# Kernel optimization log

Hardware: AMD Instinct MI355X
Metric: run time of the kernel (lower is better)

The kernel has to match this reference:

```python
import jax, jax.numpy as jnp
import numpy as np

N = 50000
E = 400000
IN_C, HID, OUT2, NCLS = 128, 512, 64, 2
NEG_SLOPE = 0.2


def setup_inputs() -> dict:
    key = jax.random.key(0)
    ks = jax.random.split(key, 12)
    x = jax.random.normal(ks[0], (N, IN_C), dtype=jnp.float32)
    edge_index = jax.random.randint(ks[1], (2, E), 0, N, dtype=jnp.int64)
    def glorot(k, shape):
        fan_in = shape[0]
        return jax.random.normal(k, shape, dtype=jnp.float32) / np.float32(np.sqrt(fan_in))
    return {
        "x": x,
        "edge_index": edge_index,
        "W1": glorot(ks[2], (IN_C, HID)),
        "a1_src": glorot(ks[3], (HID,)),
        "a1_dst": glorot(ks[4], (HID,)),
        "b1": jnp.zeros((HID,), jnp.float32),
        "W2": glorot(ks[5], (HID, OUT2)),
        "a2_src": glorot(ks[6], (OUT2,)),
        "a2_dst": glorot(ks[7], (OUT2,)),
        "b2": jnp.zeros((OUT2,), jnp.float32),
        "fcW": glorot(ks[8], (OUT2, NCLS)),
        "fcb": jnp.zeros((NCLS,), jnp.float32),
    }


def _gat_conv(h_in, src, dst, W, a_src, a_dst, b):
    # single-head GATConv (PyG defaults: heads=1, negative_slope=0.2, self-loops already added)
    h = h_in @ W                                   # [N, D]
    alpha_s = h @ a_src                            # [N]
    alpha_d = h @ a_dst                            # [N]
    e = jax.nn.leaky_relu(alpha_s[src] + alpha_d[dst], NEG_SLOPE)  # [E']
    # segment softmax over incoming edges of each dst node
    m = jax.ops.segment_max(e, dst, num_segments=N)
    ex = jnp.exp(e - m[dst])
    denom = jax.ops.segment_sum(ex, dst, num_segments=N)
    alpha = ex / denom[dst]                        # [E']
    out = jax.ops.segment_sum(alpha[:, None] * h[src], dst, num_segments=N)
    return out + b


def reference(x, edge_index, W1, a1_src, a1_dst, b1, W2, a2_src, a2_dst, b2, fcW, fcb):
    loops = jnp.arange(N, dtype=edge_index.dtype)
    src = jnp.concatenate([edge_index[0], loops])  # add self loops (PyG default)
    dst = jnp.concatenate([edge_index[1], loops])
    h = jax.nn.relu(_gat_conv(x, src, dst, W1, a1_src, a1_dst, b1))
    h = jax.nn.relu(_gat_conv(h, src, dst, W2, a2_src, a2_dst, b2))
    # F.dropout(training=self.training): identity in eval mode
    return h @ fcW + fcb
```

## Files before the change

### kernel.cpp

```cpp
#include <hip/hip_runtime.h>

#define N_NODES 50000
#define N_EDGES 400000
#define E_TOT   (N_EDGES + N_NODES)
#define IN_C 128
#define HID  512
#define OUT2 64
#define NEG_SLOPE 0.2f

typedef short bf16x8 __attribute__((ext_vector_type(8)));
typedef float f32x4  __attribute__((ext_vector_type(4)));

__device__ __forceinline__ float wave_sum(float v) {
#pragma unroll
  for (int o = 32; o > 0; o >>= 1) v += __shfl_xor(v, o, 64);
  return v;
}
__device__ __forceinline__ int wave_sum_i(int v) {
#pragma unroll
  for (int o = 32; o > 0; o >>= 1) v += __shfl_xor(v, o, 64);
  return v;
}
__device__ __forceinline__ float wave_max(float v) {
#pragma unroll
  for (int o = 32; o > 0; o >>= 1) v = fmaxf(v, __shfl_xor(v, o, 64));
  return v;
}
__device__ __forceinline__ float leaky(float t) {
  return (t > 0.f) ? t : NEG_SLOPE * t;
}

__device__ __forceinline__ unsigned short bf16_rne(float x) {
  unsigned u = __float_as_uint(x);
  u += 0x7fffu + ((u >> 16) & 1u);
  return (unsigned short)(u >> 16);
}
__device__ __forceinline__ void split_bf16(float x, unsigned short& h, unsigned short& l) {
  h = bf16_rne(x);
  float hf = __uint_as_float(((unsigned)h) << 16);
  l = bf16_rne(x - hf);
}

__device__ __forceinline__ int esrc(const int* __restrict__ ei, int e) {
  return (e < N_EDGES) ? ei[e] : (e - N_EDGES);
}
__device__ __forceinline__ int edst(const int* __restrict__ ei, int e) {
  return (e < N_EDGES) ? ei[N_EDGES + e] : (e - N_EDGES);
}

__global__ void count_deg(const int* __restrict__ ei, int* __restrict__ deg) {
  int e = blockIdx.x * blockDim.x + threadIdx.x;
  if (e >= E_TOT) return;
  atomicAdd(&deg[edst(ei, e)], 1);
}

__global__ void scanA(const int* __restrict__ deg, int* __restrict__ bsum) {
  __shared__ int ws[16];
  int t = threadIdx.x, lane = t & 63, w = t >> 6;
  int i = blockIdx.x * 1024 + t;
  int v = (i < N_NODES) ? deg[i] : 0;
  int s = wave_sum_i(v);
  if (lane == 0) ws[w] = s;
  __syncthreads();
  if (t == 0) {
    int tot = 0;
#pragma unroll
    for (int k = 0; k < 16; k++) tot += ws[k];
    bsum[blockIdx.x] = tot;
  }
}

__global__ void scanB(const int* __restrict__ bsum, int* __restrict__ boff, int nb) {
  int lane = threadIdx.x;
  int v = (lane < nb) ? bsum[lane] : 0;
  int sc = v;
#pragma unroll
  for (int off = 1; off < 64; off <<= 1) {
    int u = __shfl_up(sc, off, 64);
    if (lane >= off) sc += u;
  }
  if (lane < nb) boff[lane] = sc - v;
}

__global__ void scanC(const int* __restrict__ deg, const int* __restrict__ boff,
                      int* __restrict__ row_ptr) {
  __shared__ int ws[16];
  int t = threadIdx.x, lane = t & 63, w = t >> 6;
  int i = blockIdx.x * 1024 + t;
  int v = (i < N_NODES) ? deg[i] : 0;
  int sc = v;
#pragma unroll
  for (int off = 1; off < 64; off <<= 1) {
    int u = __shfl_up(sc, off, 64);
    if (lane >= off) sc += u;
  }
  if (lane == 63) ws[w] = sc;
  __syncthreads();
  if (w == 0 && lane < 16) {
    int u = ws[lane];
#pragma unroll
    for (int off = 1; off < 16; off <<= 1) {
      int uu = __shfl_up(u, off, 64);
      if (lane >= off) u += uu;
    }
    ws[lane] = u;
  }
  __syncthreads();
  int excl = ((w > 0) ? ws[w - 1] : 0) + boff[blockIdx.x];
  if (i < N_NODES) row_ptr[i + 1] = sc + excl;
  if (blockIdx.x == 0 && t == 0) row_ptr[0] = 0;
}

__global__ void fill_csr(const int* __restrict__ ei, const int* __restrict__ row_ptr,
                         int* __restrict__ cursor, int* __restrict__ csr_src) {
  int e = blockIdx.x * blockDim.x + threadIdx.x;
  if (e >= E_TOT) return;
  int d = edst(ei, e);
  int pos = atomicAdd(&cursor[d], 1);
  csr_src[row_ptr[d] + pos] = esrc(ei, e);
}

__global__ void prep_weights(const float* __restrict__ W1, const float* __restrict__ W2,
                             const float* __restrict__ a1s, const float* __restrict__ a1d,
                             unsigned short* __restrict__ W1F, unsigned short* __restrict__ W2F,
                             float* __restrict__ w1s, float* __restrict__ w1d) {
  int b = blockIdx.x;
  if (b < 32) {
    int t = b * 256 + threadIdx.x;
    int fi = t >> 6, l = t & 63;
    int ks = fi & 3, n = (fi >> 2) & 3, jt = fi >> 4;
    int col = jt * 64 + n * 16 + (l & 15);
    int k0 = ks * 32 + (l >> 4) * 8;
    unsigned short hv[8], lv[8];
#pragma unroll
    for (int e = 0; e < 8; e++)
      split_bf16(W1[(size_t)(k0 + e) * HID + col], hv[e], lv[e]);
    unsigned short* ph = W1F + ((size_t)(fi * 2 + 0) * 64 + l) * 8;
    unsigned short* pl = W1F + ((size_t)(fi * 2 + 1) * 64 + l) * 8;
#pragma unroll
    for (int e = 0; e < 8; e++) { ph[e] = hv[e]; pl[e] = lv[e]; }
  } else if (b < 48) {
    int t = (b - 32) * 256 + threadIdx.x;
    int fi = t >> 6, l = t & 63;
    int n = fi & 3, ks = (fi >> 2) & 1, jt = fi >> 3;
    int col = n * 16 + (l & 15);
    int k0 = jt * 64 + ks * 32 + (l >> 4) * 8;
    unsigned short hv[8], lv[8];
#pragma unroll
    for (int e = 0; e < 8; e++)
      split_bf16(W2[(size_t)(k0 + e) * OUT2 + col], hv[e], lv[e]);
    unsigned short* ph = W2F + ((size_t)(fi * 2 + 0) * 64 + l) * 8;
    unsigned short* pl = W2F + ((size_t)(fi * 2 + 1) * 64 + l) * 8;
#pragma unroll
    for (int e = 0; e < 8; e++) { ph[e] = hv[e]; pl[e] = lv[e]; }
  } else {
    int wid = ((b - 48) * 256 + threadIdx.x) >> 6;
    int lane = threadIdx.x & 63;
    if (wid >= IN_C) return;
    const float* row = W1 + (size_t)wid * HID;
    float s = 0.f, d = 0.f;
#pragma unroll
    for (int j0 = 0; j0 < HID; j0 += 64) {
      float w = row[j0 + lane];
      s += w * a1s[j0 + lane];
      d += w * a1d[j0 + lane];
    }
    s = wave_sum(s); d = wave_sum(d);
    if (lane == 0) { w1s[wid] = s; w1d[wid] = d; }
  }
}

__global__ void node_scores128(const float* __restrict__ x, const float* __restrict__ ws,
                               const float* __restrict__ wd, float* __restrict__ as_,
                               float* __restrict__ ad_) {
  int wid = (blockIdx.x * blockDim.x + threadIdx.x) >> 6;
  int lane = threadIdx.x & 63;
  if (wid >= N_NODES) return;
  float2 v = ((const float2*)(x + (size_t)wid * IN_C))[lane];
  float2 w1 = ((const float2*)ws)[lane];
  float2 w2 = ((const float2*)wd)[lane];
  float s = wave_sum(v.x * w1.x + v.y * w1.y);
  float d = wave_sum(v.x * w2.x + v.y * w2.y);
  if (lane == 0) { as_[wid] = s; ad_[wid] = d; }
}

__global__ void sm_agg1(const int* __restrict__ row_ptr, const int* __restrict__ csr_src,
                        const float* __restrict__ as_, const float* __restrict__ ad_,
                        const float* __restrict__ x, float* __restrict__ xa) {
  int wid = (blockIdx.x * blockDim.x + threadIdx.x) >> 6;
  int lane = threadIdx.x & 63;
  if (wid >= N_NODES) return;
  int beg = row_ptr[wid], end = row_ptr[wid + 1];
  int deg = end - beg;
  float adv = ad_[wid];
  const float2* x2 = (const float2*)x;
  float2 acc = make_float2(0.f, 0.f);
  if (deg <= 64) {
    int s = 0; float sc = -3.4e38f;
    if (lane < deg) { s = csr_src[beg + lane]; sc = leaky(as_[s] + adv); }
    float m = wave_max(sc);
    float ex = (lane < deg) ? __expf(sc - m) : 0.f;
    float sum = wave_sum(ex);
    float a = ex / sum;
    int kk = 0;
    for (; kk + 8 <= deg; kk += 8) {
      float w0 = __shfl(a, kk, 64),     w1 = __shfl(a, kk + 1, 64);
      float w2 = __shfl(a, kk + 2, 64), w3 = __shfl(a, kk + 3, 64);
      float w4 = __shfl(a, kk + 4, 64), w5 = __shfl(a, kk + 5, 64);
      float w6 = __shfl(a, kk + 6, 64), w7 = __shfl(a, kk + 7, 64);
      int s0 = __shfl(s, kk, 64),     s1 = __shfl(s, kk + 1, 64);
      int s2 = __shfl(s, kk + 2, 64), s3 = __shfl(s, kk + 3, 64);
      int s4 = __shfl(s, kk + 4, 64), s5 = __shfl(s, kk + 5, 64);
      int s6 = __shfl(s, kk + 6, 64), s7 = __shfl(s, kk + 7, 64);
      float2 r0 = x2[(size_t)s0 * 64 + lane];
      float2 r1 = x2[(size_t)s1 * 64 + lane];
      float2 r2 = x2[(size_t)s2 * 64 + lane];
      float2 r3 = x2[(size_t)s3 * 64 + lane];
      float2 r4 = x2[(size_t)s4 * 64 + lane];
      float2 r5 = x2[(size_t)s5 * 64 + lane];
      float2 r6 = x2[(size_t)s6 * 64 + lane];
      float2 r7 = x2[(size_t)s7 * 64 + lane];
      acc.x += w0 * r0.x + w1 * r1.x + w2 * r2.x + w3 * r3.x
             + w4 * r4.x + w5 * r5.x + w6 * r6.x + w7 * r7.x;
      acc.y += w0 * r0.y + w1 * r1.y + w2 * r2.y + w3 * r3.y
             + w4 * r4.y + w5 * r5.y + w6 * r6.y + w7 * r7.y;
    }
    for (; kk + 4 <= deg; kk += 4) {
      float w0 = __shfl(a, kk, 64),     w1 = __shfl(a, kk + 1, 64);
      float w2 = __shfl(a, kk + 2, 64), w3 = __shfl(a, kk + 3, 64);
      int s0 = __shfl(s, kk, 64),     s1 = __shfl(s, kk + 1, 64);
      int s2 = __shfl(s, kk + 2, 64), s3 = __shfl(s, kk + 3, 64);
      float2 r0 = x2[(size_t)s0 * 64 + lane];
      float2 r1 = x2[(size_t)s1 * 64 + lane];
      float2 r2 = x2[(size_t)s2 * 64 + lane];
      float2 r3 = x2[(size_t)s3 * 64 + lane];
      acc.x += w0 * r0.x + w1 * r1.x + w2 * r2.x + w3 * r3.x;
      acc.y += w0 * r0.y + w1 * r1.y + w2 * r2.y + w3 * r3.y;
    }
    for (; kk < deg; kk++) {
      float w = __shfl(a, kk, 64);
      int sv = __shfl(s, kk, 64);
      float2 r = x2[(size_t)sv * 64 + lane];
      acc.x += w * r.x; acc.y += w * r.y;
    }
  } else {
    float m = -3.4e38f;
    for (int k = beg + lane; k < end; k += 64)
      m = fmaxf(m, leaky(as_[csr_src[k]] + adv));
    m = wave_max(m);
    float sum = 0.f;
    for (int k = beg + lane; k < end; k += 64)
      sum += __expf(leaky(as_[csr_src[k]] + adv) - m);
    sum = wave_sum(sum);
    float inv = 1.f / sum;
    for (int k = beg; k < end; k++) {
      int sv = csr_src[k];
      float w = __expf(leaky(as_[sv] + adv) - m) * inv;
      float2 r = x2[(size_t)sv * 64 + lane];
      acc.x += w * r.x; acc.y += w * r.y;
    }
  }
  ((float2*)(xa + (size_t)wid * IN_C))[lane] = acc;
}

__launch_bounds__(128, 2)
__global__ void fused_gemm_mfma(const float* __restrict__ xa,
                                const unsigned short* __restrict__ W1F,
                                const float* __restrict__ b1,
                                const unsigned short* __restrict__ W2F,
                                const float* __restrict__ a2s, const float* __restrict__ a2d,
                                float* __restrict__ h2, float* __restrict__ as2,
                                float* __restrict__ ad2) {
  __shared__ unsigned int TS[64][64];
  int t = threadIdx.x;
  int w = t >> 6;
  int l = t & 63;
  int lr = l & 15;
  int G  = l >> 4;
  int base = blockIdx.x * 64 + w * 32;

  bf16x8 aFh[2][4], aFl[2][4];
#pragma unroll
  for (int m = 0; m < 2; m++) {
    int grow = base + m * 16 + lr;
    bool ok = (grow < N_NODES);
    const float* rp = xa + (size_t)grow * IN_C;
#pragma unroll
    for (int ks = 0; ks < 4; ks++) {
      float4 v0 = make_float4(0.f, 0.f, 0.f, 0.f), v1 = v0;
      if (ok) {
        v0 = *(const float4*)(rp + ks * 32 + G * 8);
        v1 = *(const float4*)(rp + ks * 32 + G * 8 + 4);
      }
      unsigned short h, lo;
      split_bf16(v0.x, h, lo); aFh[m][ks][0] = (short)h; aFl[m][ks][0] = (short)lo;
      split_bf16(v0.y, h, lo); aFh[m][ks][1] = (short)h; aFl[m][ks][1] = (short)lo;
      split_bf16(v0.z, h, lo); aFh[m][ks][2] = (short)h; aFl[m][ks][2] = (short)lo;
      split_bf16(v0.w, h, lo); aFh[m][ks][3] = (short)h; aFl[m][ks][3] = (short)lo;
      split_bf16(v1.x, h, lo); aFh[m][ks][4] = (short)h; aFl[m][ks][4] = (short)lo;
      split_bf16(v1.y, h, lo); aFh[m][ks][5] = (short)h; aFl[m][ks][5] = (short)lo;
      split_bf16(v1.z, h, lo); aFh[m][ks][6] = (short)h; aFl[m][ks][6] = (short)lo;
      split_bf16(v1.w, h, lo); aFh[m][ks][7] = (short)h; aFl[m][ks][7] = (short)lo;
    }
  }

  const bf16x8* W1Fv = (const bf16x8*)W1F;
  const bf16x8* W2Fv = (const bf16x8*)W2F;

  f32x4 acc2[2][4];
#pragma unroll
  for (int m = 0; m < 2; m++)
#pragma unroll
    for (int n = 0; n < 4; n++) acc2[m][n] = (f32x4){0.f, 0.f, 0.f, 0.f};

  for (int jt = 0; jt < 8; jt++) {
    bf16x8 w2h[2][4], w2l[2][4];
#pragma unroll
    for (int ks = 0; ks < 2; ks++)
#pragma unroll
      for (int n = 0; n < 4; n++) {
        int fi2 = (jt * 2 + ks) * 4 + n;
        w2h[ks][n] = W2Fv[(size_t)(fi2 * 2 + 0) * 64 + l];
        w2l[ks][n] = W2Fv[(size_t)(fi2 * 2 + 1) * 64 + l];
      }
    f32x4 acc1[2][4];
#pragma unroll
    for (int m = 0; m < 2; m++)
#pragma unroll
      for (int n = 0; n < 4; n++) acc1[m][n] = (f32x4){0.f, 0.f, 0.f, 0.f};
#pragma unroll
    for (int ks = 0; ks < 4; ks++) {
      bf16x8 bh[4], bl[4];
#pragma unroll
      for (int n = 0; n < 4; n++) {
        int fi = (jt * 4 + n) * 4 + ks;
        bh[n] = W1Fv[(size_t)(fi * 2 + 0) * 64 + l];
        bl[n] = W1Fv[(size_t)(fi * 2 + 1) * 64 + l];
      }
#pragma unroll
      for (int n = 0; n < 4; n++) {
#pragma unroll
        for (int m = 0; m < 2; m++) {
          acc1[m][n] = __builtin_amdgcn_mfma_f32_16x16x32_bf16(aFh[m][ks], bh[n], acc1[m][n], 0, 0, 0);
          acc1[m][n] = __builtin_amdgcn_mfma_f32_16x16x32_bf16(aFl[m][ks], bh[n], acc1[m][n], 0, 0, 0);
          acc1[m][n] = __builtin_amdgcn_mfma_f32_16x16x32_bf16(aFh[m][ks], bl[n], acc1[m][n], 0, 0, 0);
        }
      }
    }
#pragma unroll
    for (int n = 0; n < 4; n++) {
      float bv = b1[jt * 64 + n * 16 + lr];
#pragma unroll
      for (int m = 0; m < 2; m++) {
#pragma unroll
        for (int r = 0; r < 4; r++) {
          float vv = fmaxf(acc1[m][n][r] + bv, 0.f);
          unsigned short hh, ll;
          split_bf16(vv, hh, ll);
          int rowL = w * 32 + m * 16 + G * 4 + r;
          int colS = (n * 16 + lr) ^ ((rowL & 7) << 2);
          TS[rowL][colS] = (unsigned)hh | ((unsigned)ll << 16);
        }
      }
    }
#pragma unroll
    for (int ks = 0; ks < 2; ks++) {
      int kl = ks * 32 + G * 8;
      bf16x8 a2h[2], a2l[2];
#pragma unroll
      for (int m = 0; m < 2; m++) {
        int rowA = w * 32 + m * 16 + lr;
        int sw2 = (rowA & 7) << 2;
        uint4 q0 = *(const uint4*)&TS[rowA][(kl + 0) ^ sw2];
        uint4 q1 = *(const uint4*)&TS[rowA][(kl + 4) ^ sw2];
        a2h[m][0] = (short)(q0.x & 0xffff); a2l[m][0] = (short)(q0.x >> 16);
        a2h[m][1] = (short)(q0.y & 0xffff); a2l[m][1] = (short)(q0.y >> 16);
        a2h[m][2] = (short)(q0.z & 0xffff); a2l[m][2] = (short)(q0.z >> 16);
        a2h[m][3] = (short)(q0.w & 0xffff); a2l[m][3] = (short)(q0.w >> 16);
        a2h[m][4] = (short)(q1.x & 0xffff); a2l[m][4] = (short)(q1.x >> 16);
        a2h[m][5] = (short)(q1.y & 0xffff); a2l[m][5] = (short)(q1.y >> 16);
        a2h[m][6] = (short)(q1.z & 0xffff); a2l[m][6] = (short)(q1.z >> 16);
        a2h[m][7] = (short)(q1.w & 0xffff); a2l[m][7] = (short)(q1.w >> 16);
      }
#pragma unroll
      for (int n = 0; n < 4; n++) {
#pragma unroll
        for (int m = 0; m < 2; m++) {
          acc2[m][n] = __builtin_amdgcn_mfma_f32_16x16x32_bf16(a2h[m], w2h[ks][n], acc2[m][n], 0, 0, 0);
          acc2[m][n] = __builtin_amdgcn_mfma_f32_16x16x32_bf16(a2l[m], w2h[ks][n], acc2[m][n], 0, 0, 0);
          acc2[m][n] = __builtin_amdgcn_mfma_f32_16x16x32_bf16(a2h[m], w2l[ks][n], acc2[m][n], 0, 0, 0);
        }
      }
    }
  }

#pragma unroll
  for (int m = 0; m < 2; m++) {
#pragma unroll
    for (int r = 0; r < 4; r++) {
      int grow = base + m * 16 + G * 4 + r;
      if (grow < N_NODES) {
#pragma unroll
        for (int n = 0; n < 4; n++)
          h2[(size_t)grow * OUT2 + n * 16 + lr] = acc2[m][n][r];
      }
      float sp = 0.f, dp = 0.f;
#pragma unroll
      for (int n = 0; n < 4; n++) {
        float v = acc2[m][n][r];
        sp += v * a2s[n * 16 + lr];
        dp += v * a2d[n * 16 + lr];
      }
#pragma unroll
      for (int o = 1; o < 16; o <<= 1) {
        sp += __shfl_xor(sp, o, 64);
        dp += __shfl_xor(dp, o, 64);
      }
      if (lr == 0 && grow < N_NODES) { as2[grow] = sp; ad2[grow] = dp; }
    }
  }
}

__global__ void sm_agg2_final(const int* __restrict__ row_ptr, const int* __restrict__ csr_src,
                              const float* __restrict__ as_, const float* __restrict__ ad_,
                              const float* __restrict__ h2, const float* __restrict__ b2,
                              const float* __restrict__ fcW, const float* __restrict__ fcb,
                              float* __restrict__ out) {
  int wid = (blockIdx.x * blockDim.x + threadIdx.x) >> 6;
  int lane = threadIdx.x & 63;
  if (wid >= N_NODES) return;
  int beg = row_ptr[wid], end = row_ptr[wid + 1];
  int deg = end - beg;
  float adv = ad_[wid];
  float acc = 0.f;
  if (deg <= 64) {
    int s = 0; float sc = -3.4e38f;
    if (lane < deg) { s = csr_src[beg + lane]; sc = leaky(as_[s] + adv); }
    float m = wave_max(sc);
    float ex = (lane < deg) ? __expf(sc - m) : 0.f;
    float sum = wave_sum(ex);
    float a = ex / sum;
    int kk = 0;
    for (; kk + 8 <= deg; kk += 8) {
      float w0 = __shfl(a, kk, 64),     w1 = __shfl(a, kk + 1, 64);
      float w2 = __shfl(a, kk + 2, 64), w3 = __shfl(a, kk + 3, 64);
      float w4 = __shfl(a, kk + 4, 64), w5 = __shfl(a, kk + 5, 64);
      float w6 = __shfl(a, kk + 6, 64), w7 = __shfl(a, kk + 7, 64);
      int s0 = __shfl(s, kk, 64),     s1 = __shfl(s, kk + 1, 64);
      int s2 = __shfl(s, kk + 2, 64), s3 = __shfl(s, kk + 3, 64);
      int s4 = __shfl(s, kk + 4, 64), s5 = __shfl(s, kk + 5, 64);
      int s6 = __shfl(s, kk + 6, 64), s7 = __shfl(s, kk + 7, 64);
      float r0 = h2[(size_t)s0 * OUT2 + lane];
      float r1 = h2[(size_t)s1 * OUT2 + lane];
      float r2 = h2[(size_t)s2 * OUT2 + lane];
      float r3 = h2[(size_t)s3 * OUT2 + lane];
      float r4 = h2[(size_t)s4 * OUT2 + lane];
      float r5 = h2[(size_t)s5 * OUT2 + lane];
      float r6 = h2[(size_t)s6 * OUT2 + lane];
      float r7 = h2[(size_t)s7 * OUT2 + lane];
      acc += w0 * r0 + w1 * r1 + w2 * r2 + w3 * r3
           + w4 * r4 + w5 * r5 + w6 * r6 + w7 * r7;
    }
    for (; kk + 4 <= deg; kk += 4) {
      float w0 = __shfl(a, kk, 64),     w1 = __shfl(a, kk + 1, 64);
      float w2 = __shfl(a, kk + 2, 64), w3 = __shfl(a, kk + 3, 64);
      int s0 = __shfl(s, kk, 64),     s1 = __shfl(s, kk + 1, 64);
      int s2 = __shfl(s, kk + 2, 64), s3 = __shfl(s, kk + 3, 64);
      float r0 = h2[(size_t)s0 * OUT2 + lane];
      float r1 = h2[(size_t)s1 * OUT2 + lane];
      float r2 = h2[(size_t)s2 * OUT2 + lane];
      float r3 = h2[(size_t)s3 * OUT2 + lane];
      acc += w0 * r0 + w1 * r1 + w2 * r2 + w3 * r3;
    }
    for (; kk < deg; kk++) {
      float w = __shfl(a, kk, 64);
      int sv = __shfl(s, kk, 64);
      acc += w * h2[(size_t)sv * OUT2 + lane];
    }
  } else {
    float m = -3.4e38f;
    for (int k = beg + lane; k < end; k += 64)
      m = fmaxf(m, leaky(as_[csr_src[k]] + adv));
    m = wave_max(m);
    float sum = 0.f;
    for (int k = beg + lane; k < end; k += 64)
      sum += __expf(leaky(as_[csr_src[k]] + adv) - m);
    sum = wave_sum(sum);
    float inv = 1.f / sum;
    for (int k = beg; k < end; k++) {
      int sv = csr_src[k];
      float w = __expf(leaky(as_[sv] + adv) - m) * inv;
      acc += w * h2[(size_t)sv * OUT2 + lane];
    }
  }
  float v = fmaxf(acc + b2[lane], 0.f);
  float2 fw = ((const float2*)fcW)[lane];
  float f0 = wave_sum(v * fw.x);
  float f1 = wave_sum(v * fw.y);
  if (lane == 0) {
    out[(size_t)wid * 2 + 0] = f0 + fcb[0];
    out[(size_t)wid * 2 + 1] = f1 + fcb[1];
  }
}

extern "C" void kernel_launch(void* const* d_in, const int* in_sizes, int n_in,
                              void* d_out, int out_size, void* d_ws, size_t ws_size,
                              hipStream_t stream) {
  const float* x    = (const float*)d_in[0];
  const int*   ei   = (const int*)d_in[1];
  const float* W1   = (const float*)d_in[2];
  const float* a1s  = (const float*)d_in[3];
  const float* a1d  = (const float*)d_in[4];
  const float* b1   = (const float*)d_in[5];
  const float* W2   = (const float*)d_in[6];
  const float* a2s  = (const float*)d_in[7];
  const float* a2d  = (const float*)d_in[8];
  const float* b2   = (const float*)d_in[9];
  const float* fcW  = (const float*)d_in[10];
  const float* fcb  = (const float*)d_in[11];
  float* out = (float*)d_out;

  char* p = (char*)d_ws;
  float* xa    = (float*)p; p += (size_t)N_NODES * IN_C * 4;
  float* h2    = (float*)p; p += (size_t)N_NODES * OUT2 * 4;
  float* as1   = (float*)p; p += (size_t)N_NODES * 4;
  float* ad1   = (float*)p; p += (size_t)N_NODES * 4;
  float* w1s   = (float*)p; p += 256 * 4;
  float* w1d   = (float*)p; p += 256 * 4;
  int* row_ptr = (int*)p;   p += (size_t)(N_NODES + 4) * 4;
  int* deg     = (int*)p;   p += (size_t)N_NODES * 4;
  int* bsum    = (int*)p;   p += 64 * 4;
  int* boff    = (int*)p;   p += 64 * 4;
  int* csr_src = (int*)p;   p += (size_t)E_TOT * 4;
  unsigned short* W1F = (unsigned short*)p; p += (size_t)128 * 2 * 64 * 8 * 2;
  unsigned short* W2F = (unsigned short*)p; p += (size_t)64 * 2 * 64 * 8 * 2;

  const int edge_blocks = (E_TOT + 255) / 256;
  const int node_wave_blocks = (N_NODES + 3) / 4;
  const int m_tiles64 = (N_NODES + 63) / 64;
  const int scan_blocks = (N_NODES + 1023) / 1024;

  hipMemsetAsync(deg, 0, (size_t)N_NODES * 4, stream);
  count_deg<<<edge_blocks, 256, 0, stream>>>(ei, deg);
  scanA<<<scan_blocks, 1024, 0, stream>>>(deg, bsum);
  scanB<<<1, 64, 0, stream>>>(bsum, boff, scan_blocks);
  scanC<<<scan_blocks, 1024, 0, stream>>>(deg, boff, row_ptr);
  hipMemsetAsync(deg, 0, (size_t)N_NODES * 4, stream);
  fill_csr<<<edge_blocks, 256, 0, stream>>>(ei, row_ptr, deg, csr_src);
  prep_weights<<<80, 256, 0, stream>>>(W1, W2, a1s, a1d, W1F, W2F, w1s, w1d);

  node_scores128<<<node_wave_blocks, 256, 0, stream>>>(x, w1s, w1d, as1, ad1);
  sm_agg1<<<node_wave_blocks, 256, 0, stream>>>(row_ptr, csr_src, as1, ad1, x, xa);

  fused_gemm_mfma<<<m_tiles64, 128, 0, stream>>>(xa, W1F, b1, W2F,
                                                 a2s, a2d, h2, as1, ad1);

  sm_agg2_final<<<node_wave_blocks, 256, 0, stream>>>(row_ptr, csr_src, as1, ad1, h2, b2,
                                                      fcW, fcb, out);
}
```

Before: 266.9 us.

## Stage GEMM weight fragments in LDS via direct global-to-LDS loads, 128-row tiles

The fused two-layer GEMM now loads each jt-slice of W1/W2 bf16 fragments once per block into shared memory with global_load_lds, instead of each wave reading them from global memory into registers. The block grows to 4 waves covering 128 rows, so each staged weight slice is reused by more waves and fewer register-resident weight fragments are live. The CSR build also uses a separate zeroed cursor array, cleared by the same memset as deg, which drops one memset launch. The cost is two barriers per jt iteration and about 80KB of LDS per block, which may limit occupancy.

After: 256.9 us. 3.7% less time.

```diff
diff --git a/kernel.cpp b/kernel.cpp
--- a/kernel.cpp
+++ b/kernel.cpp
@@ -39,6 +39,12 @@
   h = bf16_rne(x);
   float hf = __uint_as_float(((unsigned)h) << 16);
   l = bf16_rne(x - hf);
+}
+
+__device__ __forceinline__ void gload_lds16(const void* g, void* lds) {
+  __builtin_amdgcn_global_load_lds(
+      (const __attribute__((address_space(1))) unsigned int*)g,
+      (__attribute__((address_space(3))) unsigned int*)lds, 16, 0, 0);
 }
 
 __device__ __forceinline__ int esrc(const int* __restrict__ ei, int e) {
@@ -263,7 +269,7 @@
   ((float2*)(xa + (size_t)wid * IN_C))[lane] = acc;
 }
 
-__launch_bounds__(128, 2)
+__launch_bounds__(256, 2)
 __global__ void fused_gemm_mfma(const float* __restrict__ xa,
                                 const unsigned short* __restrict__ W1F,
                                 const float* __restrict__ b1,
@@ -271,13 +277,14 @@
                                 const float* __restrict__ a2s, const float* __restrict__ a2d,
                                 float* __restrict__ h2, float* __restrict__ as2,
                                 float* __restrict__ ad2) {
-  __shared__ unsigned int TS[64][64];
+  __shared__ uint4 Bst[48 * 64];
+  __shared__ unsigned int TS[128][64];
   int t = threadIdx.x;
   int w = t >> 6;
   int l = t & 63;
   int lr = l & 15;
   int G  = l >> 4;
-  int base = blockIdx.x * 64 + w * 32;
+  int base = blockIdx.x * 128 + w * 32;
 
   bf16x8 aFh[2][4], aFl[2][4];
 #pragma unroll
@@ -304,46 +311,51 @@
     }
   }
 
-  const bf16x8* W1Fv = (const bf16x8*)W1F;
-  const bf16x8* W2Fv = (const bf16x8*)W2F;
-
   f32x4 acc2[2][4];
 #pragma unroll
   for (int m = 0; m < 2; m++)
 #pragma unroll
     for (int n = 0; n < 4; n++) acc2[m][n] = (f32x4){0.f, 0.f, 0.f, 0.f};
 
+  const char* ldsB = (const char*)&Bst[0];
+
   for (int jt = 0; jt < 8; jt++) {
-    bf16x8 w2h[2][4], w2l[2][4];
-#pragma unroll
-    for (int ks = 0; ks < 2; ks++)
+    __syncthreads();
+#pragma unroll
+    for (int i = 0; i < 12; i++) {
+      int f = w * 12 + i;
+      const char* src;
+      if (f < 32) {
+        int hl = f & 1, ks = (f >> 1) & 3, n = f >> 3;
+        int fi = (jt * 4 + n) * 4 + ks;
+        src = (const char*)W1F + ((size_t)(fi * 2 + hl) * 64 + l) * 16;
+      } else {
+        int f2 = f - 32;
+        int hl = f2 & 1, n = (f2 >> 1) & 3, ks = f2 >> 3;
+        int fi2 = (jt * 2 + ks) * 4 + n;
+        src = (const char*)W2F + ((size_t)(fi2 * 2 + hl) * 64 + l) * 16;
+      }
+      gload_lds16(src, (void*)((char*)&Bst[0] + (size_t)f * 1024));
+    }
+    __syncthreads();
+
+    f32x4 acc1[2][4];
+#pragma unroll
+    for (int m = 0; m < 2; m++)
+#pragma unroll
+      for (int n = 0; n < 4; n++) acc1[m][n] = (f32x4){0.f, 0.f, 0.f, 0.f};
+#pragma unroll
+    for (int ks = 0; ks < 4; ks++) {
 #pragma unroll
       for (int n = 0; n < 4; n++) {
-        int fi2 = (jt * 2 + ks) * 4 + n;
-        w2h[ks][n] = W2Fv[(size_t)(fi2 * 2 + 0) * 64 + l];
-        w2l[ks][n] = W2Fv[(size_t)(fi2 * 2 + 1) * 64 + l];
-      }
-    f32x4 acc1[2][4];
-#pragma unroll
-    for (int m = 0; m < 2; m++)
-#pragma unroll
-      for (int n = 0; n < 4; n++) acc1[m][n] = (f32x4){0.f, 0.f, 0.f, 0.f};
-#pragma unroll
-    for (int ks = 0; ks < 4; ks++) {
-      bf16x8 bh[4], bl[4];
-#pragma unroll
-      for (int n = 0; n < 4; n++) {
-        int fi = (jt * 4 + n) * 4 + ks;
-        bh[n] = W1Fv[(size_t)(fi * 2 + 0) * 64 + l];
-        bl[n] = W1Fv[(size_t)(fi * 2 + 1) * 64 + l];
-      }
-#pragma unroll
-      for (int n = 0; n < 4; n++) {
+        const char* bp = ldsB + (size_t)((n << 3) | (ks << 1)) * 1024 + (size_t)l * 16;
+        bf16x8 b_h = *(const bf16x8*)bp;
+        bf16x8 b_l = *(const bf16x8*)(bp + 1024);
 #pragma unroll
         for (int m = 0; m < 2; m++) {
-          acc1[m][n] = __builtin_amdgcn_mfma_f32_16x16x32_bf16(aFh[m][ks], bh[n], acc1[m][n], 0, 0, 0);
-          acc1[m][n] = __builtin_amdgcn_mfma_f32_16x16x32_bf16(aFl[m][ks], bh[n], acc1[m][n], 0, 0, 0);
-          acc1[m][n] = __builtin_amdgcn_mfma_f32_16x16x32_bf16(aFh[m][ks], bl[n], acc1[m][n], 0, 0, 0);
+          acc1[m][n] = __builtin_amdgcn_mfma_f32_16x16x32_bf16(aFh[m][ks], b_h, acc1[m][n], 0, 0, 0);
+          acc1[m][n] = __builtin_amdgcn_mfma_f32_16x16x32_bf16(aFl[m][ks], b_h, acc1[m][n], 0, 0, 0);
+          acc1[m][n] = __builtin_amdgcn_mfma_f32_16x16x32_bf16(aFh[m][ks], b_l, acc1[m][n], 0, 0, 0);
         }
       }
     }
@@ -384,11 +396,14 @@
       }
 #pragma unroll
       for (int n = 0; n < 4; n++) {
+        const char* bp = ldsB + (size_t)(32 + ((ks << 3) | (n << 1))) * 1024 + (size_t)l * 16;
+        bf16x8 b_h = *(const bf16x8*)bp;
+        bf16x8 b_l = *(const bf16x8*)(bp + 1024);
 #pragma unroll
         for (int m = 0; m < 2; m++) {
-          acc2[m][n] = __builtin_amdgcn_mfma_f32_16x16x32_bf16(a2h[m], w2h[ks][n], acc2[m][n], 0, 0, 0);
-          acc2[m][n] = __builtin_amdgcn_mfma_f32_16x16x32_bf16(a2l[m], w2h[ks][n], acc2[m][n], 0, 0, 0);
-          acc2[m][n] = __builtin_amdgcn_mfma_f32_16x16x32_bf16(a2h[m], w2l[ks][n], acc2[m][n], 0, 0, 0);
+          acc2[m][n] = __builtin_amdgcn_mfma_f32_16x16x32_bf16(a2h[m], b_h, acc2[m][n], 0, 0, 0);
+          acc2[m][n] = __builtin_amdgcn_mfma_f32_16x16x32_bf16(a2l[m], b_h, acc2[m][n], 0, 0, 0);
+          acc2[m][n] = __builtin_amdgcn_mfma_f32_16x16x32_bf16(a2h[m], b_l, acc2[m][n], 0, 0, 0);
         }
       }
     }
@@ -529,6 +544,7 @@
   float* w1d   = (float*)p; p += 256 * 4;
   int* row_ptr = (int*)p;   p += (size_t)(N_NODES + 4) * 4;
   int* deg     = (int*)p;   p += (size_t)N_NODES * 4;
+  int* cursor  = (int*)p;   p += (size_t)N_NODES * 4;
   int* bsum    = (int*)p;   p += 64 * 4;
   int* boff    = (int*)p;   p += 64 * 4;
   int* csr_src = (int*)p;   p += (size_t)E_TOT * 4;
@@ -537,23 +553,22 @@
 
   const int edge_blocks = (E_TOT + 255) / 256;
   const int node_wave_blocks = (N_NODES + 3) / 4;
-  const int m_tiles64 = (N_NODES + 63) / 64;
+  const int m_tiles128 = (N_NODES + 127) / 128;
   const int scan_blocks = (N_NODES + 1023) / 1024;
 
-  hipMemsetAsync(deg, 0, (size_t)N_NODES * 4, stream);
+  hipMemsetAsync(deg, 0, (size_t)N_NODES * 8, stream);
   count_deg<<<edge_blocks, 256, 0, stream>>>(ei, deg);
   scanA<<<scan_blocks, 1024, 0, stream>>>(deg, bsum);
   scanB<<<1, 64, 0, stream>>>(bsum, boff, scan_blocks);
   scanC<<<scan_blocks, 1024, 0, stream>>>(deg, boff, row_ptr);
-  hipMemsetAsync(deg, 0, (size_t)N_NODES * 4, stream);
-  fill_csr<<<edge_blocks, 256, 0, stream>>>(ei, row_ptr, deg, csr_src);
+  fill_csr<<<edge_blocks, 256, 0, stream>>>(ei, row_ptr, cursor, csr_src);
   prep_weights<<<80, 256, 0, stream>>>(W1, W2, a1s, a1d, W1F, W2F, w1s, w1d);
 
   node_scores128<<<node_wave_blocks, 256, 0, stream>>>(x, w1s, w1d, as1, ad1);
   sm_agg1<<<node_wave_blocks, 256, 0, stream>>>(row_ptr, csr_src, as1, ad1, x, xa);
 
-  fused_gemm_mfma<<<m_tiles64, 128, 0, stream>>>(xa, W1F, b1, W2F,
-                                                 a2s, a2d, h2, as1, ad1);
+  fused_gemm_mfma<<<m_tiles128, 256, 0, stream>>>(xa, W1F, b1, W2F,
+                                                  a2s, a2d, h2, as1, ad1);
 
   sm_agg2_final<<<node_wave_blocks, 256, 0, stream>>>(row_ptr, csr_src, as1, ad1, h2, b2,
                                                       fcW, fcb, out);
```
